# Performance work log

Hardware: AMD Instinct MI355X
Metric: run time of the kernel (lower is better)

## Reference

```python
import jax, jax.numpy as jnp
import numpy as np

N = 100000
E = 1600000
IN_C = 128
HID = 256
OUT_C = 128
MLP_H = 512  # hidden_state_factor * hidden_channels


def _mk_mlp(key, d_in, d_h, d_out):
    ks = jax.random.split(key, 3)
    s = 0.02
    return (
        jax.random.normal(ks[0], (d_in, d_h), jnp.float32) * s, jnp.zeros((d_h,), jnp.float32),
        jax.random.normal(ks[1], (d_h, d_h), jnp.float32) * s, jnp.zeros((d_h,), jnp.float32),
        jax.random.normal(ks[2], (d_h, d_out), jnp.float32) * s, jnp.zeros((d_out,), jnp.float32),
    )


def _mlp(x, w1, b1, w2, b2, w3, b3, last_act):
    h = jax.nn.relu(x @ w1 + b1)
    h = jax.nn.relu(h @ w2 + b2)
    h = h @ w3 + b3
    return jax.nn.relu(h) if last_act else h


def setup_inputs() -> dict:
    key = jax.random.key(0)
    kx, ke, k1, k2, k3 = jax.random.split(key, 5)
    x = jax.random.normal(kx, (N, IN_C), jnp.float32)
    edge_index = jax.random.randint(ke, (2, E), 0, N, jnp.int64)
    enc = _mk_mlp(k1, IN_C, MLP_H, HID)
    conv = _mk_mlp(k2, HID, MLP_H, HID)
    dec = _mk_mlp(k3, HID, MLP_H, OUT_C)
    names_enc = ["enc_w1", "enc_b1", "enc_w2", "enc_b2", "enc_w3", "enc_b3"]
    names_conv = ["conv_w1", "conv_b1", "conv_w2", "conv_b2", "conv_w3", "conv_b3"]
    names_dec = ["dec_w1", "dec_b1", "dec_w2", "dec_b2", "dec_w3", "dec_b3"]
    d = {"x": x, "edge_index": edge_index, "iterations": 1}
    d.update(dict(zip(names_enc, enc)))
    d.update(dict(zip(names_conv, conv)))
    d.update(dict(zip(names_dec, dec)))
    return d


def reference(x, edge_index,
              enc_w1, enc_b1, enc_w2, enc_b2, enc_w3, enc_b3,
              conv_w1, conv_b1, conv_w2, conv_b2, conv_w3, conv_b3,
              dec_w1, dec_b1, dec_w2, dec_b2, dec_w3, dec_b3,
              iterations):
    # encoder MLP (Identity norm, ReLU, dropout=0)
    h = _mlp(x, enc_w1, enc_b1, enc_w2, enc_b2, enc_w3, enc_b3, True)  # [N, HID]
    # GINConv: scatter-add neighbor features (eps=0): agg[i] = sum_{j->i} h[j]
    src, dst = edge_index[0], edge_index[1]
    agg = jax.ops.segment_sum(h[src], dst, num_segments=h.shape[0])  # [N, HID]
    # residual: x = x + conv_mlp(h + agg)
    h = h + _mlp(h + agg, conv_w1, conv_b1, conv_w2, conv_b2, conv_w3, conv_b3, True)
    # decoder MLP without last activation
    return _mlp(h, dec_w1, dec_b1, dec_w2, dec_b2, dec_w3, dec_b3, False)
```

## Files before the change

kernel.cpp:

```cpp
#include <hip/hip_runtime.h>
#include <cstdint>
#include <cstddef>


typedef __attribute__((ext_vector_type(8))) __bf16 bf16x8;
typedef __attribute__((ext_vector_type(4))) float f32x4;

__device__ __forceinline__ unsigned short f2bf(float f) {
    unsigned int u = __float_as_uint(f);
    u += 0x7FFF + ((u >> 16) & 1);
    return (unsigned short)(u >> 16);
}
__device__ __forceinline__ float bf2f(unsigned int s) {
    return __uint_as_float(s << 16);
}

template<bool RELU, bool HAS_RES, bool SF32, bool ORDER>
__global__ __launch_bounds__(256, 4)
void gemm128(const unsigned short* __restrict__ A,
             const unsigned short* __restrict__ Wt,
             const float* __restrict__ Bias,
             const unsigned short* __restrict__ Res,
             float* __restrict__ Cf, unsigned short* __restrict__ Cb,
             int M, int K, int N, int MT, int orderBlocks,
             const int* __restrict__ ei, int* __restrict__ cur,
             int* __restrict__ ssrc, int E)
{
    __shared__ unsigned short As[128 * 64];
    __shared__ unsigned short Bs[128 * 64];

    const int tid  = threadIdx.x;

    if (ORDER && (int)blockIdx.x < orderBlocks) {
        const int nth = orderBlocks * 256;
        for (int e = (int)blockIdx.x * 256 + tid; e < E; e += nth) {
            const int s = ei[e];
            const int d = ei[E + e];
            const int pos = atomicAdd(&cur[d], 1);
            ssrc[pos] = s;
        }
        return;
    }

    const int bid = ORDER ? ((int)blockIdx.x - orderBlocks) : (int)blockIdx.x;
    const int mtile = bid % MT;
    const int ntile = bid / MT;
    const int m0 = mtile * 128;
    const int n0 = ntile * 128;

    const int wave = tid >> 6;
    const int lane = tid & 63;
    const int wm = wave >> 1;
    const int wn = wave & 1;

    f32x4 acc[4][4];
#pragma unroll
    for (int i = 0; i < 4; ++i)
#pragma unroll
        for (int j = 0; j < 4; ++j) acc[i][j] = (f32x4){0.f, 0.f, 0.f, 0.f};

    const int srow = (wave << 5) + (lane >> 3);
    const int scol = (lane & 7) << 3;

    for (int k0 = 0; k0 < K; k0 += 64) {
#pragma unroll
        for (int i = 0; i < 4; ++i) {
            const int row = srow + i * 8;
            int gm = m0 + row; gm = (gm < M) ? gm : (M - 1);
            const unsigned short* gp = A + (size_t)gm * K + k0 + scol;
            __builtin_amdgcn_global_load_lds(
                (const __attribute__((address_space(1))) void*)gp,
                (__attribute__((address_space(3))) void*)&As[(wave * 2048) + i * 512],
                16, 0, 0);
        }
#pragma unroll
        for (int i = 0; i < 4; ++i) {
            const int row = srow + i * 8;
            const unsigned short* gp = Wt + (size_t)(n0 + row) * K + k0 + scol;
            __builtin_amdgcn_global_load_lds(
                (const __attribute__((address_space(1))) void*)gp,
                (__attribute__((address_space(3))) void*)&Bs[(wave * 2048) + i * 512],
                16, 0, 0);
        }
        asm volatile("s_waitcnt vmcnt(0)" ::: "memory");
        __syncthreads();

        const int lr = lane & 15;
        const int lk = (lane >> 4) << 3;
#pragma unroll
        for (int kk = 0; kk < 64; kk += 32) {
            bf16x8 af[4], bg[4];
#pragma unroll
            for (int f = 0; f < 4; ++f) {
                af[f] = *(const bf16x8*)&As[(wm * 64 + f * 16 + lr) * 64 + kk + lk];
                bg[f] = *(const bf16x8*)&Bs[(wn * 64 + f * 16 + lr) * 64 + kk + lk];
            }
#pragma unroll
            for (int mf = 0; mf < 4; ++mf)
#pragma unroll
                for (int nf = 0; nf < 4; ++nf)
                    acc[mf][nf] = __builtin_amdgcn_mfma_f32_16x16x32_bf16(
                        af[mf], bg[nf], acc[mf][nf], 0, 0, 0);
        }
        __syncthreads();
    }

    const int lr = lane & 15;
    const int lg = lane >> 4;
#pragma unroll
    for (int mf = 0; mf < 4; ++mf) {
#pragma unroll
        for (int r = 0; r < 4; ++r) {
            const int row = m0 + wm * 64 + mf * 16 + lg * 4 + r;
            if (row >= M) continue;
#pragma unroll
            for (int nf = 0; nf < 4; ++nf) {
                const int col = n0 + wn * 64 + nf * 16 + lr;
                float v = acc[mf][nf][r] + Bias[col];
                if (RELU) v = fmaxf(v, 0.f);
                if (HAS_RES) v += bf2f(Res[(size_t)row * N + col]);
                if (SF32) Cf[(size_t)row * N + col] = v;
                else      Cb[(size_t)row * N + col] = f2bf(v);
            }
        }
    }
}

struct PrepArgs {
    const float* W[9];
    unsigned short* Wt[9];
    int wstart[10];
    int Kd[9], Nd[9];
    const float* x;
    unsigned short* xbf;
    const int* ei;
    int* cnt;
    int histBlocks, wtTotal, nCvt4, E;
};

__global__ __launch_bounds__(256)
void prep_kernel(PrepArgs a)
{
    __shared__ unsigned short t[64][72];
    int b = blockIdx.x;
    const int tid = threadIdx.x;
    if (b < a.histBlocks) {
        const int nth = a.histBlocks * 256;
        for (int e = b * 256 + tid; e < a.E; e += nth)
            atomicAdd(&a.cnt[a.ei[a.E + e]], 1);
        return;
    }
    b -= a.histBlocks;
    if (b < a.wtTotal) {
        int job = 0;
        while (b >= a.wstart[job + 1]) ++job;
        const int lb = b - a.wstart[job];
        const int K = a.Kd[job], N = a.Nd[job];
        const int kt = K >> 6;
        const int kb = (lb % kt) * 64, nb = (lb / kt) * 64;
        const float* W = a.W[job];
        unsigned short* Wt = a.Wt[job];
        const int kl = tid >> 4, n4 = (tid & 15) << 2;
#pragma unroll
        for (int it = 0; it < 4; ++it) {
            const int k = kl + it * 16;
            const float4 v = *(const float4*)&W[(size_t)(kb + k) * N + nb + n4];
            t[n4 + 0][k] = f2bf(v.x); t[n4 + 1][k] = f2bf(v.y);
            t[n4 + 2][k] = f2bf(v.z); t[n4 + 3][k] = f2bf(v.w);
        }
        __syncthreads();
        const int n = tid >> 2, kc = (tid & 3) << 4;
        *(uint4*)&Wt[(size_t)(nb + n) * K + kb + kc]     = *(const uint4*)&t[n][kc];
        *(uint4*)&Wt[(size_t)(nb + n) * K + kb + kc + 8] = *(const uint4*)&t[n][kc + 8];
        return;
    }
    b -= a.wtTotal;
    const int i = b * 256 + tid;
    if (i < a.nCvt4) {
        const float4 v = ((const float4*)a.x)[i];
        ushort4 o;
        o.x = f2bf(v.x); o.y = f2bf(v.y); o.z = f2bf(v.z); o.w = f2bf(v.w);
        ((ushort4*)a.xbf)[i] = o;
    }
}

__global__ __launch_bounds__(256)
void zero_ints(int* __restrict__ p, int n)
{
    const int i = blockIdx.x * 256 + threadIdx.x;
    if (i < n) p[i] = 0;
}

__global__ __launch_bounds__(256)
void scan_reduce(const int* __restrict__ cnt, int* __restrict__ bsum, int N)
{
    __shared__ int s[256];
    const int i = blockIdx.x * 256 + threadIdx.x;
    s[threadIdx.x] = (i < N) ? cnt[i] : 0;
    __syncthreads();
#pragma unroll
    for (int off = 128; off > 0; off >>= 1) {
        if (threadIdx.x < off) s[threadIdx.x] += s[threadIdx.x + off];
        __syncthreads();
    }
    if (threadIdx.x == 0) bsum[blockIdx.x] = s[0];
}

__global__ __launch_bounds__(512)
void scan_blocksums(int* __restrict__ bsum, int NB)
{
    __shared__ int a[512], b[512];
    const int t = threadIdx.x;
    const int v = (t < NB) ? bsum[t] : 0;
    a[t] = v;
    __syncthreads();
    int* s = a; int* d = b;
    for (int off = 1; off < 512; off <<= 1) {
        int x = s[t];
        if (t >= off) x += s[t - off];
        d[t] = x;
        __syncthreads();
        int* tmp = s; s = d; d = tmp;
    }
    if (t < NB) bsum[t] = s[t] - v;
}

__global__ __launch_bounds__(256)
void scan_final(const int* __restrict__ cnt, const int* __restrict__ bpre,
                int* __restrict__ off, int* __restrict__ cur, int N)
{
    __shared__ int a[256], b[256];
    const int i = blockIdx.x * 256 + threadIdx.x;
    const int t = threadIdx.x;
    const int v = (i < N) ? cnt[i] : 0;
    a[t] = v;
    __syncthreads();
    int* s = a; int* d = b;
    for (int o = 1; o < 256; o <<= 1) {
        int x = s[t];
        if (t >= o) x += s[t - o];
        d[t] = x;
        __syncthreads();
        int* tmp = s; s = d; d = tmp;
    }
    const int excl = s[t] - v + bpre[blockIdx.x];
    if (i < N) {
        off[i] = excl;
        cur[i] = excl;
        if (i == N - 1) off[N] = excl + v;
    }
}

__global__ __launch_bounds__(256)
void agg_kernel(const unsigned short* __restrict__ hbf, const int* __restrict__ off,
                const int* __restrict__ ssrc, unsigned short* __restrict__ hpg, int Nn)
{
    const int gw   = (int)((blockIdx.x * 256 + threadIdx.x) >> 6);
    const int lane = threadIdx.x & 63;
    const int node = gw >> 1;
    if (node >= Nn) return;
    const int ci = (gw & 1) * 64 + lane;
    const int e0 = off[node], e1 = off[node + 1];
    const unsigned int* base = (const unsigned int*)hbf;

    unsigned int u = base[(size_t)node * 128 + ci];
    float a0 = bf2f(u & 0xffffu), a1 = bf2f(u >> 16);

    int e = e0;
    for (; e + 7 < e1; e += 8) {
        int s[8];
#pragma unroll
        for (int j = 0; j < 8; ++j) s[j] = ssrc[e + j];
        unsigned int v[8];
#pragma unroll
        for (int j = 0; j < 8; ++j) v[j] = base[(size_t)s[j] * 128 + ci];
#pragma unroll
        for (int j = 0; j < 8; ++j) {
            a0 += bf2f(v[j] & 0xffffu);
            a1 += bf2f(v[j] >> 16);
        }
    }
    for (; e + 1 < e1; e += 2) {
        const unsigned int v0 = base[(size_t)ssrc[e]     * 128 + ci];
        const unsigned int v1 = base[(size_t)ssrc[e + 1] * 128 + ci];
        a0 += bf2f(v0 & 0xffffu) + bf2f(v1 & 0xffffu);
        a1 += bf2f(v0 >> 16)     + bf2f(v1 >> 16);
    }
    if (e < e1) {
        const unsigned int v0 = base[(size_t)ssrc[e] * 128 + ci];
        a0 += bf2f(v0 & 0xffffu); a1 += bf2f(v0 >> 16);
    }
    ((unsigned int*)hpg)[(size_t)node * 128 + ci] =
        (unsigned)f2bf(a0) | ((unsigned)f2bf(a1) << 16);
}


extern "C" void kernel_launch(void* const* d_in, const int* in_sizes, int n_in,
                              void* d_out, int out_size, void* d_ws, size_t ws_size,
                              hipStream_t stream)
{
    const float* x  = (const float*)d_in[0];
    const int*   ei = (const int*)d_in[1];
    const float* W[9]  = {(const float*)d_in[3],  (const float*)d_in[5],  (const float*)d_in[7],
                          (const float*)d_in[9],  (const float*)d_in[11], (const float*)d_in[13],
                          (const float*)d_in[15], (const float*)d_in[17], (const float*)d_in[19]};
    const float* B[9]  = {(const float*)d_in[4],  (const float*)d_in[6],  (const float*)d_in[8],
                          (const float*)d_in[10], (const float*)d_in[12], (const float*)d_in[14],
                          (const float*)d_in[16], (const float*)d_in[18], (const float*)d_in[20]};
    const int    Kd[9] = {128, 512, 512, 256, 512, 512, 256, 512, 512};
    const int    Nd[9] = {512, 512, 256, 512, 512, 256, 512, 512, 128};
    float* out = (float*)d_out;

    const int M = 100000;
    const int E = 1600000;
    const size_t HN = (size_t)M * 256;
    const int ORDER_BLOCKS = 768;
    const int HIST_BLOCKS  = 1024;

    char* p = (char*)d_ws;
    auto carve = [&](size_t bytes) -> char* {
        char* r = p;
        p += (bytes + 255) & ~(size_t)255;
        return r;
    };
    unsigned short* hbf   = (unsigned short*)carve(HN * 2);
    unsigned short* hpgbf = (unsigned short*)carve(HN * 2);
    unsigned short* xbf   = (unsigned short*)carve((size_t)M * 128 * 2);
    unsigned short* Wt[9];
    for (int i = 0; i < 9; ++i) Wt[i] = (unsigned short*)carve((size_t)Kd[i] * Nd[i] * 2);
    int* cnt  = (int*)carve(M * 4);
    int* off  = (int*)carve((M + 4) * 4);
    int* cur  = (int*)carve(M * 4);
    int* bsum = (int*)carve(512 * 4);
    int* ssrc = (int*)carve((size_t)E * 4);

    const size_t fixed = (size_t)(p - (char*)d_ws);
    size_t remain = (ws_size > fixed) ? ws_size - fixed : 0;
    size_t cap = remain / (2 * 512 * 2);
    if (cap < 4096) cap = 4096;
    const int nch = (cap >= (size_t)M) ? 1 : (int)((M + cap - 1) / cap);
    const int CH = (M + nch - 1) / nch;
    unsigned short* t1 = (unsigned short*)carve((size_t)CH * 512 * 2);
    unsigned short* t2 = (unsigned short*)carve((size_t)CH * 512 * 2);

    const dim3 blk(256);
    const int NB = (M + 255) / 256;

    zero_ints<<<NB, blk, 0, stream>>>(cnt, M);

    PrepArgs pa;
    pa.wstart[0] = 0;
    for (int i = 0; i < 9; ++i) {
        pa.W[i] = W[i]; pa.Wt[i] = Wt[i]; pa.Kd[i] = Kd[i]; pa.Nd[i] = Nd[i];
        pa.wstart[i + 1] = pa.wstart[i] + (Kd[i] / 64) * (Nd[i] / 64);
    }
    pa.x = x; pa.xbf = xbf; pa.ei = ei; pa.cnt = cnt;
    pa.histBlocks = HIST_BLOCKS;
    pa.wtTotal = pa.wstart[9];
    pa.nCvt4 = M * 128 / 4;
    pa.E = E;
    const int cvtBlocks = (pa.nCvt4 + 255) / 256;
    prep_kernel<<<HIST_BLOCKS + pa.wtTotal + cvtBlocks, blk, 0, stream>>>(pa);

    scan_reduce<<<NB, blk, 0, stream>>>(cnt, bsum, M);
    scan_blocksums<<<1, 512, 0, stream>>>(bsum, NB);
    scan_final<<<NB, blk, 0, stream>>>(cnt, bsum, off, cur, M);

    auto mt = [](int m) { return (m + 127) / 128; };

    for (int m0 = 0; m0 < M; m0 += CH) {
        const int cm = (M - m0 < CH) ? (M - m0) : CH;
        const int MT = mt(cm);
        gemm128<true, false, false, false><<<MT * 4, blk, 0, stream>>>(
            xbf + (size_t)m0 * 128, Wt[0], B[0], nullptr, nullptr, t1,
            cm, 128, 512, MT, 0, nullptr, nullptr, nullptr, 0);
        if (m0 == 0) {
            gemm128<true, false, false, true><<<ORDER_BLOCKS + MT * 4, blk, 0, stream>>>(
                t1, Wt[1], B[1], nullptr, nullptr, t2, cm, 512, 512, MT,
                ORDER_BLOCKS, ei, cur, ssrc, E);
        } else {
            gemm128<true, false, false, false><<<MT * 4, blk, 0, stream>>>(
                t1, Wt[1], B[1], nullptr, nullptr, t2, cm, 512, 512, MT,
                0, nullptr, nullptr, nullptr, 0);
        }
        gemm128<true, false, false, false><<<MT * 2, blk, 0, stream>>>(
            t2, Wt[2], B[2], nullptr, nullptr, hbf + (size_t)m0 * 256, cm, 512, 256, MT,
            0, nullptr, nullptr, nullptr, 0);
    }

    agg_kernel<<<(int)(((size_t)2 * M * 64 + 255) / 256), blk, 0, stream>>>(
        hbf, off, ssrc, hpgbf, M);

    for (int m0 = 0; m0 < M; m0 += CH) {
        const int cm = (M - m0 < CH) ? (M - m0) : CH;
        const int MT = mt(cm);
        gemm128<true, false, false, false><<<MT * 4, blk, 0, stream>>>(
            hpgbf + (size_t)m0 * 256, Wt[3], B[3], nullptr, nullptr, t1, cm, 256, 512, MT,
            0, nullptr, nullptr, nullptr, 0);
        gemm128<true, false, false, false><<<MT * 4, blk, 0, stream>>>(
            t1, Wt[4], B[4], nullptr, nullptr, t2, cm, 512, 512, MT,
            0, nullptr, nullptr, nullptr, 0);
        gemm128<true, true, false, false><<<MT * 2, blk, 0, stream>>>(
            t2, Wt[5], B[5], hbf + (size_t)m0 * 256, nullptr, hpgbf + (size_t)m0 * 256,
            cm, 512, 256, MT, 0, nullptr, nullptr, nullptr, 0);
    }

    for (int m0 = 0; m0 < M; m0 += CH) {
        const int cm = (M - m0 < CH) ? (M - m0) : CH;
        const int MT = mt(cm);
        gemm128<true, false, false, false><<<MT * 4, blk, 0, stream>>>(
            hpgbf + (size_t)m0 * 256, Wt[6], B[6], nullptr, nullptr, t1, cm, 256, 512, MT,
            0, nullptr, nullptr, nullptr, 0);
        gemm128<true, false, false, false><<<MT * 4, blk, 0, stream>>>(
            t1, Wt[7], B[7], nullptr, nullptr, t2, cm, 512, 512, MT,
            0, nullptr, nullptr, nullptr, 0);
        gemm128<false, false, true, false><<<MT, blk, 0, stream>>>(
            t2, Wt[8], B[8], nullptr, out + (size_t)m0 * 128, nullptr, cm, 512, 128, MT,
            0, nullptr, nullptr, nullptr, 0);
    }
}
```

Baseline: 937.3 us.

## Double-buffer GEMM LDS tiles with async prefetch and XOR-swizzled layout

The GEMM mainloop now keeps two LDS buffers for A and B and issues the global-to-LDS loads for the next K tile before computing on the current one. A partial vmcnt wait lets those loads overlap the MFMA work. The source column is XOR-swizzled by row so the fragment reads avoid LDS bank conflicts. Shared memory per block doubles, and launch bounds drop from 4 to 2 blocks per SM, which lowers occupancy.

```diff
diff --git a/kernel.cpp b/kernel.cpp
--- a/kernel.cpp
+++ b/kernel.cpp
@@ -15,8 +15,10 @@
     return __uint_as_float(s << 16);
 }
 
+#define FENCE asm volatile("" ::: "memory")
+
 template<bool RELU, bool HAS_RES, bool SF32, bool ORDER>
-__global__ __launch_bounds__(256, 4)
+__global__ __launch_bounds__(256, 2)
 void gemm128(const unsigned short* __restrict__ A,
              const unsigned short* __restrict__ Wt,
              const float* __restrict__ Bias,
@@ -26,8 +28,8 @@
              const int* __restrict__ ei, int* __restrict__ cur,
              int* __restrict__ ssrc, int E)
 {
-    __shared__ unsigned short As[128 * 64];
-    __shared__ unsigned short Bs[128 * 64];
+    __shared__ unsigned short As[2][128 * 64];
+    __shared__ unsigned short Bs[2][128 * 64];
 
     const int tid  = threadIdx.x;
 
@@ -60,9 +62,9 @@
         for (int j = 0; j < 4; ++j) acc[i][j] = (f32x4){0.f, 0.f, 0.f, 0.f};
 
     const int srow = (wave << 5) + (lane >> 3);
-    const int scol = (lane & 7) << 3;
-
-    for (int k0 = 0; k0 < K; k0 += 64) {
+    const int scol = (((lane & 7) ^ (lane >> 3)) << 3);
+
+    auto stage = [&](int buf, int k0) {
 #pragma unroll
         for (int i = 0; i < 4; ++i) {
             const int row = srow + i * 8;
@@ -70,7 +72,7 @@
             const unsigned short* gp = A + (size_t)gm * K + k0 + scol;
             __builtin_amdgcn_global_load_lds(
                 (const __attribute__((address_space(1))) void*)gp,
-                (__attribute__((address_space(3))) void*)&As[(wave * 2048) + i * 512],
+                (__attribute__((address_space(3))) void*)&As[buf][(wave * 2048) + i * 512],
                 16, 0, 0);
         }
 #pragma unroll
@@ -79,21 +81,37 @@
             const unsigned short* gp = Wt + (size_t)(n0 + row) * K + k0 + scol;
             __builtin_amdgcn_global_load_lds(
                 (const __attribute__((address_space(1))) void*)gp,
-                (__attribute__((address_space(3))) void*)&Bs[(wave * 2048) + i * 512],
+                (__attribute__((address_space(3))) void*)&Bs[buf][(wave * 2048) + i * 512],
                 16, 0, 0);
         }
-        asm volatile("s_waitcnt vmcnt(0)" ::: "memory");
-        __syncthreads();
-
-        const int lr = lane & 15;
-        const int lk = (lane >> 4) << 3;
-#pragma unroll
-        for (int kk = 0; kk < 64; kk += 32) {
+    };
+
+    const int KT = K >> 6;
+    const int lr  = lane & 15;
+    const int lkw = lane >> 4;
+
+    stage(0, 0);
+
+    int buf = 0;
+    for (int t = 0; t < KT; ++t) {
+        if (t + 1 < KT) {
+            stage(buf ^ 1, (t + 1) << 6);
+            asm volatile("s_waitcnt vmcnt(8)" ::: "memory");
+        } else {
+            asm volatile("s_waitcnt vmcnt(0)" ::: "memory");
+        }
+        FENCE; __builtin_amdgcn_s_barrier(); FENCE;
+
+#pragma unroll
+        for (int kk = 0; kk < 2; ++kk) {
+            const int c16 = kk * 4 + lkw;
             bf16x8 af[4], bg[4];
 #pragma unroll
             for (int f = 0; f < 4; ++f) {
-                af[f] = *(const bf16x8*)&As[(wm * 64 + f * 16 + lr) * 64 + kk + lk];
-                bg[f] = *(const bf16x8*)&Bs[(wn * 64 + f * 16 + lr) * 64 + kk + lk];
+                const int ra = wm * 64 + f * 16 + lr;
+                af[f] = *(const bf16x8*)&As[buf][ra * 64 + ((c16 ^ (ra & 7)) << 3)];
+                const int rb = wn * 64 + f * 16 + lr;
+                bg[f] = *(const bf16x8*)&Bs[buf][rb * 64 + ((c16 ^ (rb & 7)) << 3)];
             }
 #pragma unroll
             for (int mf = 0; mf < 4; ++mf)
@@ -102,10 +120,11 @@
                     acc[mf][nf] = __builtin_amdgcn_mfma_f32_16x16x32_bf16(
                         af[mf], bg[nf], acc[mf][nf], 0, 0, 0);
         }
-        __syncthreads();
-    }
-
-    const int lr = lane & 15;
+
+        FENCE; __builtin_amdgcn_s_barrier(); FENCE;
+        buf ^= 1;
+    }
+
     const int lg = lane >> 4;
 #pragma unroll
     for (int mf = 0; mf < 4; ++mf) {
```

After: 1.072 ms. 1.14x slower.
